# Optimization experiments

Measured on AMD Instinct MI355X. Metric: run time of the kernel, lower is better.

## Reference

```python
import jax, jax.numpy as jnp
import numpy as np

N = 4096      # nodes / sequence length
E = 131072    # edges (avg degree 32)
DIN = 512     # input feature dim
D = 256       # hidden_dim == output_dim (d_model)
H = 2         # nhead
DFF = 2048    # TransformerEncoderLayer default dim_feedforward
EPS = 1e-5


def setup_inputs() -> dict:
    key = jax.random.key(0)
    ks = jax.random.split(key, 16)
    s = lambda k, shape, scale: jax.random.normal(k, shape, jnp.float32) * scale
    return {
        "x": jax.random.normal(ks[0], (N, DIN), jnp.float32),
        "edge_index": jax.random.randint(ks[1], (2, E), 0, N),
        "edge_weight": jax.random.uniform(ks[2], (E,), jnp.float32),
        "W_gcn": s(ks[3], (DIN, D), 1.0 / np.sqrt(DIN)),
        "b_gcn": jnp.zeros((D,), jnp.float32),
        "in_proj_w": s(ks[4], (3 * D, D), 1.0 / np.sqrt(D)),
        "in_proj_b": jnp.zeros((3 * D,), jnp.float32),
        "out_proj_w": s(ks[5], (D, D), 1.0 / np.sqrt(D)),
        "out_proj_b": jnp.zeros((D,), jnp.float32),
        "lin1_w": s(ks[6], (DFF, D), 1.0 / np.sqrt(D)),
        "lin1_b": jnp.zeros((DFF,), jnp.float32),
        "lin2_w": s(ks[7], (D, DFF), 1.0 / np.sqrt(DFF)),
        "lin2_b": jnp.zeros((D,), jnp.float32),
        "ln1_g": jnp.ones((D,), jnp.float32),
        "ln1_b": jnp.zeros((D,), jnp.float32),
        "ln2_g": jnp.ones((D,), jnp.float32),
        "ln2_b": jnp.zeros((D,), jnp.float32),
    }


def _layernorm(x, g, b):
    mu = jnp.mean(x, axis=-1, keepdims=True)
    var = jnp.mean(jnp.square(x - mu), axis=-1, keepdims=True)
    return (x - mu) * jax.lax.rsqrt(var + EPS) * g + b


def _gcn_conv(x, edge_index, edge_weight, W, b):
    # PyG GCNConv: linear transform, add self-loops (weight 1), symmetric
    # degree normalization, scatter-add aggregation at target nodes.
    loops = jnp.arange(N)
    src = jnp.concatenate([edge_index[0], loops])
    dst = jnp.concatenate([edge_index[1], loops])
    w = jnp.concatenate([edge_weight, jnp.ones((N,), edge_weight.dtype)])
    deg = jax.ops.segment_sum(w, dst, num_segments=N)
    dinv = jnp.where(deg > 0, jax.lax.rsqrt(deg), 0.0)
    norm = dinv[src] * w * dinv[dst]                        # [E+N]
    xw = x @ W                                              # [N, D]
    out = jax.ops.segment_sum(norm[:, None] * xw[src], dst, num_segments=N)
    return out + b


def _mha(x, in_w, in_b, out_w, out_b):
    dh = D // H
    qkv = x @ in_w.T + in_b                                 # [N, 3D]
    q, k, v = jnp.split(qkv, 3, axis=-1)
    q = q.reshape(N, H, dh)
    k = k.reshape(N, H, dh)
    v = v.reshape(N, H, dh)
    scores = jnp.einsum("qhd,khd->hqk", q, k) / np.sqrt(dh)  # [H, N, N]
    attn = jax.nn.softmax(scores, axis=-1)
    o = jnp.einsum("hqk,khd->qhd", attn, v).reshape(N, D)
    return o @ out_w.T + out_b


def reference(x, edge_index, edge_weight, W_gcn, b_gcn, in_proj_w, in_proj_b,
              out_proj_w, out_proj_b, lin1_w, lin1_b, lin2_w, lin2_b,
              ln1_g, ln1_b, ln2_g, ln2_b):
    h = jax.nn.relu(_gcn_conv(x, edge_index, edge_weight, W_gcn, b_gcn))
    # TransformerEncoderLayer, post-norm (norm_first=False), dropout=eval
    h = _layernorm(h + _mha(h, in_proj_w, in_proj_b, out_proj_w, out_proj_b),
                   ln1_g, ln1_b)
    ff = jax.nn.relu(h @ lin1_w.T + lin1_b) @ lin2_w.T + lin2_b
    return _layernorm(h + ff, ln2_g, ln2_b)
```

## Files before the change

kernel.cpp:

```cpp
#include <hip/hip_runtime.h>
#include <hip/hip_bf16.h>

#define N_NODES 4096
#define E_EDGES 131072
#define DIN_    512
#define DM_     256
#define DFF_    2048
#define EPS_    1e-5f
#define NSPLIT  8

typedef __attribute__((ext_vector_type(8))) short bf16x8;
typedef __attribute__((ext_vector_type(4))) float f32x4;

__device__ __forceinline__ short f2b(float f) {
    union { float f; unsigned u; } x; x.f = f;
    unsigned r = x.u + 0x7fff + ((x.u >> 16) & 1);
    return (short)(r >> 16);
}

__device__ __forceinline__ void gload16(const void* g, void* l) {
    __builtin_amdgcn_global_load_lds(
        (const __attribute__((address_space(1))) void*)g,
        (__attribute__((address_space(3))) void*)l, 16, 0, 0);
}

__global__ __launch_bounds__(256)
void castall_kernel(const float* __restrict__ x, short* __restrict__ xb,
                    const float* __restrict__ inw, short* __restrict__ inwb,
                    const float* __restrict__ ow, short* __restrict__ owb,
                    const float* __restrict__ l1w, short* __restrict__ l1wb,
                    const float* __restrict__ l2w, short* __restrict__ l2wb,
                    const float* __restrict__ Wg, short* __restrict__ WgT) {
    const int b = blockIdx.x;
    __shared__ float t[32][33];
    if (b >= 3328) {
        const int b2 = b - 3328;
        const int bk = (b2 & 15) * 32, bn = (b2 >> 4) * 32;
        const int tx = threadIdx.x & 31, ty = threadIdx.x >> 5;
        #pragma unroll
        for (int i = 0; i < 4; ++i) {
            int r = ty + i * 8;
            t[r][tx] = Wg[(size_t)(bk + r) * DM_ + bn + tx];
        }
        __syncthreads();
        #pragma unroll
        for (int i = 0; i < 4; ++i) {
            int r = ty + i * 8;
            WgT[(size_t)(bn + r) * DIN_ + bk + tx] = f2b(t[tx][r]);
        }
        return;
    }
    const float* s; short* d; int base;
    if (b < 2048)      { s = x;   d = xb;   base = b * 256; }
    else if (b < 2240) { s = inw; d = inwb; base = (b - 2048) * 256; }
    else if (b < 2304) { s = ow;  d = owb;  base = (b - 2240) * 256; }
    else if (b < 2816) { s = l1w; d = l1wb; base = (b - 2304) * 256; }
    else               { s = l2w; d = l2wb; base = (b - 2816) * 256; }
    const int i = base + threadIdx.x;
    float4 v = reinterpret_cast<const float4*>(s)[i];
    union { short s[4]; int2 v; } o;
    o.s[0] = f2b(v.x); o.s[1] = f2b(v.y); o.s[2] = f2b(v.z); o.s[3] = f2b(v.w);
    reinterpret_cast<int2*>(d)[i] = o.v;
}

template<int MT, bool BF16OUT, bool RELU, bool SPLITK>
__global__ __launch_bounds__(256)
void mgemm_kernel(const short* __restrict__ A, const short* __restrict__ B,
                  const float* __restrict__ bias,
                  float* __restrict__ Cf, short* __restrict__ Cb,
                  short* __restrict__ VTout,
                  int M, int N, int K, int lda, int ldb, int ldc, int kchunk)
{
    constexpr int MFN = MT / 32;
    constexpr int ACH = MT / 64;
    __shared__ __align__(16) short As[2][MT * 32];
    __shared__ __align__(16) short Bs[2][128 * 32];
    const int tid = threadIdx.x;
    const int lane = tid & 63, w = tid >> 6;
    const int c = lane & 15, g = lane >> 4;
    const int wm = (w >> 1) * (MT / 2), wn = (w & 1) * 64;
    const int bm = blockIdx.y * MT, bn = blockIdx.x * 128;
    int k0 = 0, kend = K;
    if (SPLITK) { k0 = blockIdx.z * kchunk; kend = min(K, k0 + kchunk); }

    const int wbase = (tid & ~63) * 16;
    int srowA[ACH], soffA[ACH];
    #pragma unroll
    for (int i = 0; i < ACH; ++i) {
        int L = i * 256 + tid;
        srowA[i] = L >> 2;
        soffA[i] = ((L & 3) ^ ((srowA[i] >> 1) & 3)) * 8;
    }
    int srowB[2], soffB[2];
    #pragma unroll
    for (int i = 0; i < 2; ++i) {
        int L = i * 256 + tid;
        srowB[i] = L >> 2;
        soffB[i] = ((L & 3) ^ ((srowB[i] >> 1) & 3)) * 8;
    }

    auto stage = [&](int b, int kb) {
        #pragma unroll
        for (int i = 0; i < ACH; ++i)
            gload16(A + (size_t)(bm + srowA[i]) * lda + kb + soffA[i],
                    (char*)As[b] + i * 4096 + wbase);
        #pragma unroll
        for (int i = 0; i < 2; ++i)
            gload16(B + (size_t)(bn + srowB[i]) * ldb + kb + soffB[i],
                    (char*)Bs[b] + i * 4096 + wbase);
    };

    const int nsteps = (kend - k0) >> 5;
    f32x4 acc[MFN][4] = {};
    stage(0, k0);
    for (int s = 0; s < nsteps; ++s) {
        const int cur = s & 1;
        const bool pf = (s + 1 < nsteps);
        if (pf) stage(cur ^ 1, k0 + (s + 1) * 32);
        if (pf) {
            if constexpr (ACH == 2) asm volatile("s_waitcnt vmcnt(4)" ::: "memory");
            else                    asm volatile("s_waitcnt vmcnt(3)" ::: "memory");
        } else {
            asm volatile("s_waitcnt vmcnt(0)" ::: "memory");
        }
        __builtin_amdgcn_s_barrier();
        bf16x8 af[MFN], bf[4];
        #pragma unroll
        for (int mf = 0; mf < MFN; ++mf) {
            int r = wm + mf * 16 + c;
            int sw = (g ^ ((r >> 1) & 3)) * 16;
            af[mf] = *reinterpret_cast<const bf16x8*>((const char*)As[cur] + r * 64 + sw);
        }
        #pragma unroll
        for (int nf = 0; nf < 4; ++nf) {
            int r = wn + nf * 16 + c;
            int sw = (g ^ ((r >> 1) & 3)) * 16;
            bf[nf] = *reinterpret_cast<const bf16x8*>((const char*)Bs[cur] + r * 64 + sw);
        }
        #pragma unroll
        for (int mf = 0; mf < MFN; ++mf)
            #pragma unroll
            for (int nf = 0; nf < 4; ++nf)
                acc[mf][nf] = __builtin_amdgcn_mfma_f32_16x16x32_bf16(
                    af[mf], bf[nf], acc[mf][nf], 0, 0, 0);
        __builtin_amdgcn_s_barrier();
    }
    #pragma unroll
    for (int mf = 0; mf < MFN; ++mf) {
        const int row = bm + wm + mf * 16 + g * 4;
        #pragma unroll
        for (int nf = 0; nf < 4; ++nf) {
            const int col = bn + wn + nf * 16 + c;
            float bv = bias ? bias[col] : 0.f;
            #pragma unroll
            for (int v = 0; v < 4; ++v) {
                float val = acc[mf][nf][v];
                size_t o = (size_t)(row + v) * ldc + col;
                if (SPLITK) {
                    if (blockIdx.z == 0) val += bv;
                    atomicAdd(&Cf[o], val);
                } else {
                    val += bv;
                    if (RELU) val = fmaxf(val, 0.f);
                    if (BF16OUT) {
                        short bvs = f2b(val);
                        Cb[o] = bvs;
                        if (VTout && col >= 512)
                            VTout[(size_t)(col - 512) * N_NODES + row + v] = bvs;
                    } else {
                        Cf[o] = val;
                    }
                }
            }
        }
    }
}

__global__ __launch_bounds__(256)
void fattn_kernel(const short* __restrict__ qkv, const short* __restrict__ VT,
                  short* __restrict__ Opart, float* __restrict__ ml)
{
    const int bid = blockIdx.x;
    const int j = bid >> 3;
    const int pair = 2 * (bid & 7) + (j & 1);
    const int hd = pair >> 3, sp = pair & 7;
    const int qt = j >> 1;
    const int tid = threadIdx.x;
    const int w = tid >> 6, lane = tid & 63;
    const int c = lane & 15, g = lane >> 4;
    const int q0 = qt * 64 + w * 16;

    __shared__ __align__(16) char smem[40960];
    char* KldsB = smem;
    char* VldsB = smem + 16384;
    char* Pbase = smem + 32768 + w * 2048;

    const char* qkvC = (const char*)qkv;
    const char* vtC  = (const char*)VT;
    const int wbase = (tid & ~63) * 16;

    const short* Q = qkv + (size_t)q0 * 768 + hd * 128;
    bf16x8 qf[4];
    #pragma unroll
    for (int ks = 0; ks < 4; ++ks)
        qf[ks] = *reinterpret_cast<const bf16x8*>(Q + (size_t)c * 768 + ks * 32 + g * 8);

    auto stageK = [&](int kt) {
        const int key0 = kt * 64;
        #pragma unroll
        for (int i = 0; i < 4; ++i) {
            int Lr  = i * 4096 + tid * 16;
            int key = Lr >> 8;
            int lg  = (Lr & 255) ^ ((key & 7) << 4);
            const char* src = qkvC + ((size_t)(key0 + key) * 768 + 256 + hd * 128) * 2 + lg;
            gload16(src, KldsB + i * 4096 + wbase);
        }
    };
    auto stageV = [&](int kt) {
        const int key0 = kt * 64;
        #pragma unroll
        for (int i = 0; i < 4; ++i) {
            int Lr = i * 4096 + tid * 16;
            int dh = Lr >> 7;
            int lg = (Lr & 127) ^ ((dh & 7) << 4);
            const char* src = vtC + (size_t)(hd * 128 + dh) * 8192 + key0 * 2 + lg;
            gload16(src, VldsB + i * 4096 + wbase);
        }
    };

    f32x4 O[8] = {};
    float m[4]  = {-1e30f, -1e30f, -1e30f, -1e30f};
    float lsum[4] = {};
    const float C = 0.12751744f;

    stageK(sp * 8);
    stageV(sp * 8);

    for (int t = 0; t < 8; ++t) {
        asm volatile("s_waitcnt vmcnt(4)" ::: "memory");
        __builtin_amdgcn_s_barrier();
        f32x4 S[4] = {};
        #pragma unroll
        for (int nf = 0; nf < 4; ++nf) {
            const int key = nf * 16 + c;
            const char* kr = KldsB + key * 256;
            const int sw = (key & 7) << 4;
            #pragma unroll
            for (int ks = 0; ks < 4; ++ks) {
                bf16x8 kf = *reinterpret_cast<const bf16x8*>(kr + ((ks * 64 + g * 16) ^ sw));
                S[nf] = __builtin_amdgcn_mfma_f32_16x16x32_bf16(qf[ks], kf, S[nf], 0, 0, 0);
            }
        }
        __builtin_amdgcn_s_barrier();
        if (t < 7) stageK(sp * 8 + t + 1);

        float z[4][4];
        float lmax[4];
        bool ok = true;
        #pragma unroll
        for (int v = 0; v < 4; ++v) {
            #pragma unroll
            for (int nf = 0; nf < 4; ++nf) z[nf][v] = S[nf][v] * C;
            lmax[v] = fmaxf(fmaxf(z[0][v], z[1][v]), fmaxf(z[2][v], z[3][v]));
            ok = ok && (lmax[v] <= m[v] + 8.f);
        }
        if (!__all(ok)) {
            float mx[4];
            #pragma unroll
            for (int v = 0; v < 4; ++v) mx[v] = lmax[v];
            #pragma unroll
            for (int off = 1; off <= 8; off <<= 1)
                #pragma unroll
                for (int v = 0; v < 4; ++v) mx[v] = fmaxf(mx[v], __shfl_xor(mx[v], off));
            #pragma unroll
            for (int v = 0; v < 4; ++v) {
                float mn = fmaxf(m[v], mx[v]);
                float scl = exp2f(m[v] - mn);
                m[v] = mn;
                lsum[v] *= scl;
                #pragma unroll
                for (int nf2 = 0; nf2 < 8; ++nf2) O[nf2][v] *= scl;
            }
        }
        #pragma unroll
        for (int nf = 0; nf < 4; ++nf)
            #pragma unroll
            for (int v = 0; v < 4; ++v) {
                float p = exp2f(z[nf][v] - m[v]);
                lsum[v] += p;
                union { float f; unsigned u; } pu; pu.f = p;
                const int row = 4 * g + v;
                const int bo = (row * 128 + (nf * 16 + c) * 2) ^ ((row & 7) << 4);
                *(short*)(Pbase + bo) = (short)(pu.u >> 16);
            }
        if (t < 7) asm volatile("s_waitcnt vmcnt(4)" ::: "memory");
        else       asm volatile("s_waitcnt vmcnt(0)" ::: "memory");
        __builtin_amdgcn_s_barrier();
        bf16x8 pa[2];
        #pragma unroll
        for (int ks = 0; ks < 2; ++ks) {
            const int bo = (c * 128 + ks * 64 + g * 16) ^ ((c & 7) << 4);
            pa[ks] = *reinterpret_cast<const bf16x8*>(Pbase + bo);
        }
        #pragma unroll
        for (int nf2 = 0; nf2 < 8; ++nf2) {
            const int dh = nf2 * 16 + c;
            const char* vr = VldsB + dh * 128;
            const int sw = (dh & 7) << 4;
            #pragma unroll
            for (int ks = 0; ks < 2; ++ks) {
                bf16x8 vf = *reinterpret_cast<const bf16x8*>(vr + ((ks * 64 + g * 16) ^ sw));
                O[nf2] = __builtin_amdgcn_mfma_f32_16x16x32_bf16(pa[ks], vf, O[nf2], 0, 0, 0);
            }
        }
        __builtin_amdgcn_s_barrier();
        if (t < 7) stageV(sp * 8 + t + 1);
    }
    #pragma unroll
    for (int off = 1; off <= 8; off <<= 1)
        #pragma unroll
        for (int v = 0; v < 4; ++v) lsum[v] += __shfl_xor(lsum[v], off);
    const size_t pbase = ((size_t)hd * NSPLIT + sp) * N_NODES;
    #pragma unroll
    for (int v = 0; v < 4; ++v) {
        const int row = q0 + 4 * g + v;
        const size_t rowo = (pbase + row) * 128;
        #pragma unroll
        for (int nf2 = 0; nf2 < 8; ++nf2)
            Opart[rowo + nf2 * 16 + c] = f2b(O[nf2][v]);
        if (c == 0) {
            ml[(pbase + row) * 2 + 0] = m[v];
            ml[(pbase + row) * 2 + 1] = lsum[v];
        }
    }
}

__global__ __launch_bounds__(256)
void attn_combine_kernel(const short* __restrict__ Opart, const float* __restrict__ ml,
                         short* __restrict__ attnb)
{
    const int row = blockIdx.x;
    const int hd = threadIdx.x >> 7, d = threadIdx.x & 127;
    float ms[NSPLIT], ls[NSPLIT];
    float mmax = -1e30f;
    #pragma unroll
    for (int s = 0; s < NSPLIT; ++s) {
        const size_t p = ((size_t)hd * NSPLIT + s) * N_NODES + row;
        ms[s] = ml[p * 2 + 0];
        ls[s] = ml[p * 2 + 1];
        mmax = fmaxf(mmax, ms[s]);
    }
    float lt = 0.f, acc = 0.f;
    #pragma unroll
    for (int s = 0; s < NSPLIT; ++s) {
        const float wgt = exp2f(ms[s] - mmax);
        lt += wgt * ls[s];
        const size_t p = ((size_t)hd * NSPLIT + s) * N_NODES + row;
        union { short s; unsigned short u; } b; b.s = Opart[p * 128 + d];
        union { unsigned u; float f; } cv; cv.u = ((unsigned)b.u) << 16;
        acc += wgt * cv.f;
    }
    attnb[(size_t)row * DM_ + hd * 128 + d] = f2b(acc / lt);
}

__global__ void deg_accum_kernel(const int* __restrict__ dst,
                                 const float* __restrict__ w,
                                 float* deg, int* count) {
    int e = blockIdx.x * 256 + threadIdx.x;
    if (e < E_EDGES) {
        int d = dst[e];
        atomicAdd(&deg[d], w[e]);
        atomicAdd(&count[d], 1);
    }
}
__global__ __launch_bounds__(1024)
void csr_scan_kernel(const int* __restrict__ count, int* __restrict__ start,
                     int* __restrict__ cursor, float* __restrict__ deg) {
    __shared__ int sum[1024];
    const int tid = threadIdx.x;
    const int base = tid * 4;
    #pragma unroll
    for (int i = 0; i < 4; ++i) {
        int n = base + i;
        deg[n] = rsqrtf(deg[n] + 1.0f);
    }
    int loc[4]; int s = 0;
    #pragma unroll
    for (int i = 0; i < 4; ++i) { loc[i] = count[base + i]; s += loc[i]; }
    sum[tid] = s;
    __syncthreads();
    for (int off = 1; off < 1024; off <<= 1) {
        int v = (tid >= off) ? sum[tid - off] : 0;
        __syncthreads();
        sum[tid] += v;
        __syncthreads();
    }
    int run = sum[tid] - s;
    #pragma unroll
    for (int i = 0; i < 4; ++i) {
        start[base + i] = run;
        cursor[base + i] = run;
        run += loc[i];
    }
    if (tid == 1023) start[N_NODES] = run;
}
__global__ void csr_fill_kernel(const int* __restrict__ src, const int* __restrict__ dst,
                                const float* __restrict__ w, const float* __restrict__ dinv,
                                int* __restrict__ cursor,
                                int* __restrict__ csr_src, float* __restrict__ csr_nrm) {
    int e = blockIdx.x * 256 + threadIdx.x;
    if (e >= E_EDGES) return;
    int s = src[e], d = dst[e];
    int pos = atomicAdd(&cursor[d], 1);
    csr_src[pos] = s;
    csr_nrm[pos] = dinv[s] * w[e] * dinv[d];
}
__global__ __launch_bounds__(256)
void gcn_gather_kernel(const int* __restrict__ start, const int* __restrict__ csr_src,
                       const float* __restrict__ csr_nrm, const short* __restrict__ xwb,
                       const float* __restrict__ dinv, const float* __restrict__ b,
                       float* __restrict__ h, short* __restrict__ hb) {
    const int n = blockIdx.x, tid = threadIdx.x;
    const int q = tid >> 6, lane = tid & 63;
    const int s0 = start[n], s1 = start[n + 1];
    __shared__ int    ssrc[256];
    __shared__ float  snrm[256];
    __shared__ float4 red[4][64];
    float4 acc = {0.f, 0.f, 0.f, 0.f};
    for (int base = s0; base < s1; base += 256) {
        const int cnt = min(256, s1 - base);
        __syncthreads();
        if (tid < cnt) { ssrc[tid] = csr_src[base + tid]; snrm[tid] = csr_nrm[base + tid]; }
        __syncthreads();
        for (int j = q; j < cnt; j += 4) {
            const int2 pv = *reinterpret_cast<const int2*>(
                xwb + (size_t)ssrc[j] * DM_ + lane * 4);
            union { int i; float f; } e0, e1, e2, e3;
            e0.i = pv.x << 16; e1.i = pv.x & 0xffff0000;
            e2.i = pv.y << 16; e3.i = pv.y & 0xffff0000;
            const float wj = snrm[j];
            acc.x = fmaf(wj, e0.f, acc.x);
            acc.y = fmaf(wj, e1.f, acc.y);
            acc.z = fmaf(wj, e2.f, acc.z);
            acc.w = fmaf(wj, e3.f, acc.w);
        }
    }
    red[q][lane] = acc;
    __syncthreads();
    if (q == 0) {
        const float4 a1 = red[1][lane], a2 = red[2][lane], a3 = red[3][lane];
        const float di = dinv[n], d2 = di * di;
        const int2 pv = *reinterpret_cast<const int2*>(
            xwb + (size_t)n * DM_ + lane * 4);
        union { int i; float f; } x0, x1, x2, x3;
        x0.i = pv.x << 16; x1.i = pv.x & 0xffff0000;
        x2.i = pv.y << 16; x3.i = pv.y & 0xffff0000;
        const float4 bv = *reinterpret_cast<const float4*>(b + lane * 4);
        float v0 = fmaxf(acc.x + a1.x + a2.x + a3.x + d2 * x0.f + bv.x, 0.f);
        float v1 = fmaxf(acc.y + a1.y + a2.y + a3.y + d2 * x1.f + bv.y, 0.f);
        float v2 = fmaxf(acc.z + a1.z + a2.z + a3.z + d2 * x2.f + bv.z, 0.f);
        float v3 = fmaxf(acc.w + a1.w + a2.w + a3.w + d2 * x3.f + bv.w, 0.f);
        const size_t o = (size_t)n * DM_ + lane * 4;
        *reinterpret_cast<float4*>(h + o) = make_float4(v0, v1, v2, v3);
        union { short s[4]; int2 v; } ob;
        ob.s[0] = f2b(v0); ob.s[1] = f2b(v1); ob.s[2] = f2b(v2); ob.s[3] = f2b(v3);
        *reinterpret_cast<int2*>(hb + o) = ob.v;
    }
}

__global__ __launch_bounds__(256)
void ln_kernel(const float* __restrict__ a, const float* __restrict__ b,
               const float* __restrict__ g, const float* __restrict__ be,
               float* __restrict__ outf, short* __restrict__ outb,
               float* __restrict__ clearbuf) {
    const int n = blockIdx.x, d = threadIdx.x;
    const size_t idx = (size_t)n * DM_ + d;
    float x = a[idx] + b[idx];
    if (clearbuf) clearbuf[idx] = 0.f;
    float s = x;
    #pragma unroll
    for (int off = 32; off; off >>= 1) s += __shfl_xor(s, off);
    __shared__ float red[8];
    const int wid = d >> 6;
    if ((d & 63) == 0) red[wid] = s;
    __syncthreads();
    float mu = (red[0] + red[1] + red[2] + red[3]) * (1.f / 256.f);
    float c = x - mu;
    float q = c * c;
    #pragma unroll
    for (int off = 32; off; off >>= 1) q += __shfl_xor(q, off);
    if ((d & 63) == 0) red[4 + wid] = q;
    __syncthreads();
    float var = (red[4] + red[5] + red[6] + red[7]) * (1.f / 256.f);
    float v = c * rsqrtf(var + EPS_) * g[d] + be[d];
    outf[idx] = v;
    if (outb) outb[idx] = f2b(v);
}

extern "C" void kernel_launch(void* const* d_in, const int* in_sizes, int n_in,
                              void* d_out, int out_size, void* d_ws, size_t ws_size,
                              hipStream_t stream) {
    const float* x   = (const float*)d_in[0];
    const int*   ei  = (const int*)  d_in[1];
    const float* ew  = (const float*)d_in[2];
    const float* Wg  = (const float*)d_in[3];
    const float* bg  = (const float*)d_in[4];
    const float* inw = (const float*)d_in[5];
    const float* inb = (const float*)d_in[6];
    const float* ow  = (const float*)d_in[7];
    const float* ob  = (const float*)d_in[8];
    const float* l1w = (const float*)d_in[9];
    const float* l1b = (const float*)d_in[10];
    const float* l2w = (const float*)d_in[11];
    const float* l2b = (const float*)d_in[12];
    const float* g1  = (const float*)d_in[13];
    const float* b1  = (const float*)d_in[14];
    const float* g2  = (const float*)d_in[15];
    const float* b2  = (const float*)d_in[16];
    float* out = (float*)d_out;

    char* ws = (char*)d_ws;
    size_t off = 0;
    auto alloc = [&](size_t bytes) {
        void* p = ws + off;
        off += (bytes + 255) & ~(size_t)255;
        return p;
    };
    float* deg   = (float*)alloc((size_t)N_NODES * 4);
    int*   count = (int*)  alloc((size_t)N_NODES * 4);
    size_t zspan = off;
    float* tmp     = (float*)alloc((size_t)N_NODES * DM_ * 4);
    int*   startA  = (int*)  alloc((size_t)(N_NODES + 1) * 4);
    int*   cursor  = (int*)  alloc((size_t)N_NODES * 4);
    int*   csr_src = (int*)  alloc((size_t)E_EDGES * 4);
    float* csr_nrm = (float*)alloc((size_t)E_EDGES * 4);
    short* xb    = (short*)alloc((size_t)N_NODES * DIN_ * 2);
    short* WgT   = (short*)alloc((size_t)DM_ * DIN_ * 2);
    short* inwb  = (short*)alloc((size_t)768 * DM_ * 2);
    short* owb   = (short*)alloc((size_t)DM_ * DM_ * 2);
    short* l1wb  = (short*)alloc((size_t)DFF_ * DM_ * 2);
    short* l2wb  = (short*)alloc((size_t)DM_ * DFF_ * 2);
    short* xwb   = (short*)alloc((size_t)N_NODES * DM_ * 2);
    float* h     = (float*)alloc((size_t)N_NODES * DM_ * 4);
    short* hb    = (short*)alloc((size_t)N_NODES * DM_ * 2);
    short* qkvb  = (short*)alloc((size_t)N_NODES * 768 * 2);
    short* VT    = (short*)alloc((size_t)DM_ * N_NODES * 2);
    short* attnb = (short*)alloc((size_t)N_NODES * DM_ * 2);
    float* h1    = (float*)alloc((size_t)N_NODES * DM_ * 4);
    short* h1b   = (short*)alloc((size_t)N_NODES * DM_ * 2);
    size_t opart_b = (size_t)2 * NSPLIT * N_NODES * 128 * 2;
    size_t ml_b    = (size_t)2 * NSPLIT * N_NODES * 2 * 4;
    size_t ff1_b   = (size_t)N_NODES * DFF_ * 2;
    char*  R     = (char*)alloc(opart_b + ml_b > ff1_b ? opart_b + ml_b : ff1_b);
    short* Opart = (short*)R;
    float* ml    = (float*)(R + opart_b);
    short* ff1b  = (short*)R;
    (void)ws_size; (void)in_sizes; (void)n_in; (void)out_size;

    const int* srcI = ei;
    const int* dstI = ei + E_EDGES;

    hipMemsetAsync(ws, 0, zspan, stream);
    castall_kernel<<<3456, 256, 0, stream>>>(x, xb, inw, inwb, ow, owb,
                                             l1w, l1wb, l2w, l2wb, Wg, WgT);

    deg_accum_kernel<<<E_EDGES / 256, 256, 0, stream>>>(dstI, ew, deg, count);
    csr_scan_kernel<<<1, 1024, 0, stream>>>(count, startA, cursor, deg);
    csr_fill_kernel<<<E_EDGES / 256, 256, 0, stream>>>(srcI, dstI, ew, deg, cursor,
                                                       csr_src, csr_nrm);
    mgemm_kernel<64, true, false, false><<<dim3(2, 64), 256, 0, stream>>>(
        xb, WgT, nullptr, nullptr, xwb, nullptr,
        N_NODES, DM_, DIN_, DIN_, DIN_, DM_, 0);
    gcn_gather_kernel<<<N_NODES, 256, 0, stream>>>(startA, csr_src, csr_nrm, xwb,
                                                   deg, bg, h, hb);

    mgemm_kernel<64, true, false, false><<<dim3(6, 64), 256, 0, stream>>>(
        hb, inwb, inb, nullptr, qkvb, VT,
        N_NODES, 768, DM_, DM_, DM_, 768, 0);

    fattn_kernel<<<1024, 256, 0, stream>>>(qkvb, VT, Opart, ml);
    attn_combine_kernel<<<N_NODES, 256, 0, stream>>>(Opart, ml, attnb);

    mgemm_kernel<64, false, false, false><<<dim3(2, 64), 256, 0, stream>>>(
        attnb, owb, ob, tmp, nullptr, nullptr,
        N_NODES, DM_, DM_, DM_, DM_, DM_, 0);
    ln_kernel<<<N_NODES, 256, 0, stream>>>(h, tmp, g1, b1, h1, h1b, tmp);

    mgemm_kernel<128, true, true, false><<<dim3(16, 32), 256, 0, stream>>>(
        h1b, l1wb, l1b, nullptr, ff1b, nullptr,
        N_NODES, DFF_, DM_, DM_, DM_, DFF_, 0);
    mgemm_kernel<64, false, false, true><<<dim3(2, 64, 2), 256, 0, stream>>>(
        ff1b, l2wb, l2b, tmp, nullptr, nullptr,
        N_NODES, DM_, DFF_, DFF_, DFF_, DM_, 1024);
    ln_kernel<<<N_NODES, 256, 0, stream>>>(h1, tmp, g2, b2, out, nullptr, nullptr);
}
```

Measured before the change: 173.8 us.

## Drop fp32 residual copies, use wave-per-node GCN gather, fold zeroing into cast

Rewrites the GCN gather so each wavefront handles one node with 4-way unrolled independent loads, removing LDS staging, block-wide syncs and the cross-wave reduction. The fp32 h and h1 buffers are dropped: the layernorm kernels now read the residual from the bf16 copies, which saves global writes and reads at some cost in precision. The memset of deg/count is replaced by an extra block in the cast kernel, removing one launch. The residual path now carries bf16 rounding error that the reference does not have.

```diff
diff --git a/kernel.cpp b/kernel.cpp
--- a/kernel.cpp
+++ b/kernel.cpp
@@ -17,6 +17,10 @@
     unsigned r = x.u + 0x7fff + ((x.u >> 16) & 1);
     return (short)(r >> 16);
 }
+__device__ __forceinline__ float b2f(short s) {
+    union { int i; float f; } v; v.i = ((int)(unsigned short)s) << 16;
+    return v.f;
+}
 
 __device__ __forceinline__ void gload16(const void* g, void* l) {
     __builtin_amdgcn_global_load_lds(
@@ -30,9 +34,18 @@
                     const float* __restrict__ ow, short* __restrict__ owb,
                     const float* __restrict__ l1w, short* __restrict__ l1wb,
                     const float* __restrict__ l2w, short* __restrict__ l2wb,
-                    const float* __restrict__ Wg, short* __restrict__ WgT) {
+                    const float* __restrict__ Wg, short* __restrict__ WgT,
+                    float* __restrict__ deg, int* __restrict__ count) {
     const int b = blockIdx.x;
     __shared__ float t[32][33];
+    if (b == 3456) {
+        #pragma unroll
+        for (int i = 0; i < 16; ++i) {
+            deg[threadIdx.x * 16 + i] = 0.f;
+            count[threadIdx.x * 16 + i] = 0;
+        }
+        return;
+    }
     if (b >= 3328) {
         const int b2 = b - 3328;
         const int bk = (b2 & 15) * 32, bn = (b2 >> 4) * 32;
@@ -419,63 +432,66 @@
 void gcn_gather_kernel(const int* __restrict__ start, const int* __restrict__ csr_src,
                        const float* __restrict__ csr_nrm, const short* __restrict__ xwb,
                        const float* __restrict__ dinv, const float* __restrict__ b,
-                       float* __restrict__ h, short* __restrict__ hb) {
-    const int n = blockIdx.x, tid = threadIdx.x;
-    const int q = tid >> 6, lane = tid & 63;
+                       short* __restrict__ hb) {
+    const int w = threadIdx.x >> 6, lane = threadIdx.x & 63;
+    const int n = blockIdx.x * 4 + w;
     const int s0 = start[n], s1 = start[n + 1];
-    __shared__ int    ssrc[256];
-    __shared__ float  snrm[256];
-    __shared__ float4 red[4][64];
+    const int col = lane * 4;
     float4 acc = {0.f, 0.f, 0.f, 0.f};
-    for (int base = s0; base < s1; base += 256) {
-        const int cnt = min(256, s1 - base);
-        __syncthreads();
-        if (tid < cnt) { ssrc[tid] = csr_src[base + tid]; snrm[tid] = csr_nrm[base + tid]; }
-        __syncthreads();
-        for (int j = q; j < cnt; j += 4) {
-            const int2 pv = *reinterpret_cast<const int2*>(
-                xwb + (size_t)ssrc[j] * DM_ + lane * 4);
+    int j = s0;
+    for (; j + 4 <= s1; j += 4) {
+        int   sj[4]; float wj[4]; int2 vj[4];
+        #pragma unroll
+        for (int u = 0; u < 4; ++u) { sj[u] = csr_src[j + u]; wj[u] = csr_nrm[j + u]; }
+        #pragma unroll
+        for (int u = 0; u < 4; ++u)
+            vj[u] = *reinterpret_cast<const int2*>(xwb + (size_t)sj[u] * DM_ + col);
+        #pragma unroll
+        for (int u = 0; u < 4; ++u) {
             union { int i; float f; } e0, e1, e2, e3;
-            e0.i = pv.x << 16; e1.i = pv.x & 0xffff0000;
-            e2.i = pv.y << 16; e3.i = pv.y & 0xffff0000;
-            const float wj = snrm[j];
-            acc.x = fmaf(wj, e0.f, acc.x);
-            acc.y = fmaf(wj, e1.f, acc.y);
-            acc.z = fmaf(wj, e2.f, acc.z);
-            acc.w = fmaf(wj, e3.f, acc.w);
-        }
-    }
-    red[q][lane] = acc;
-    __syncthreads();
-    if (q == 0) {
-        const float4 a1 = red[1][lane], a2 = red[2][lane], a3 = red[3][lane];
-        const float di = dinv[n], d2 = di * di;
-        const int2 pv = *reinterpret_cast<const int2*>(
-            xwb + (size_t)n * DM_ + lane * 4);
-        union { int i; float f; } x0, x1, x2, x3;
-        x0.i = pv.x << 16; x1.i = pv.x & 0xffff0000;
-        x2.i = pv.y << 16; x3.i = pv.y & 0xffff0000;
-        const float4 bv = *reinterpret_cast<const float4*>(b + lane * 4);
-        float v0 = fmaxf(acc.x + a1.x + a2.x + a3.x + d2 * x0.f + bv.x, 0.f);
-        float v1 = fmaxf(acc.y + a1.y + a2.y + a3.y + d2 * x1.f + bv.y, 0.f);
-        float v2 = fmaxf(acc.z + a1.z + a2.z + a3.z + d2 * x2.f + bv.z, 0.f);
-        float v3 = fmaxf(acc.w + a1.w + a2.w + a3.w + d2 * x3.f + bv.w, 0.f);
-        const size_t o = (size_t)n * DM_ + lane * 4;
-        *reinterpret_cast<float4*>(h + o) = make_float4(v0, v1, v2, v3);
-        union { short s[4]; int2 v; } ob;
-        ob.s[0] = f2b(v0); ob.s[1] = f2b(v1); ob.s[2] = f2b(v2); ob.s[3] = f2b(v3);
-        *reinterpret_cast<int2*>(hb + o) = ob.v;
-    }
+            e0.i = vj[u].x << 16; e1.i = vj[u].x & 0xffff0000;
+            e2.i = vj[u].y << 16; e3.i = vj[u].y & 0xffff0000;
+            acc.x = fmaf(wj[u], e0.f, acc.x);
+            acc.y = fmaf(wj[u], e1.f, acc.y);
+            acc.z = fmaf(wj[u], e2.f, acc.z);
+            acc.w = fmaf(wj[u], e3.f, acc.w);
+        }
+    }
+    for (; j < s1; ++j) {
+        const int sj = csr_src[j];
+        const float wj = csr_nrm[j];
+        const int2 v = *reinterpret_cast<const int2*>(xwb + (size_t)sj * DM_ + col);
+        union { int i; float f; } e0, e1, e2, e3;
+        e0.i = v.x << 16; e1.i = v.x & 0xffff0000;
+        e2.i = v.y << 16; e3.i = v.y & 0xffff0000;
+        acc.x = fmaf(wj, e0.f, acc.x);
+        acc.y = fmaf(wj, e1.f, acc.y);
+        acc.z = fmaf(wj, e2.f, acc.z);
+        acc.w = fmaf(wj, e3.f, acc.w);
+    }
+    const float di = dinv[n], d2 = di * di;
+    const int2 pv = *reinterpret_cast<const int2*>(xwb + (size_t)n * DM_ + col);
+    union { int i; float f; } x0, x1, x2, x3;
+    x0.i = pv.x << 16; x1.i = pv.x & 0xffff0000;
+    x2.i = pv.y << 16; x3.i = pv.y & 0xffff0000;
+    const float4 bv = *reinterpret_cast<const float4*>(b + col);
+    float v0 = fmaxf(acc.x + d2 * x0.f + bv.x, 0.f);
+    float v1 = fmaxf(acc.y + d2 * x1.f + bv.y, 0.f);
+    float v2 = fmaxf(acc.z + d2 * x2.f + bv.z, 0.f);
+    float v3 = fmaxf(acc.w + d2 * x3.f + bv.w, 0.f);
+    union { short s[4]; int2 v; } ob;
+    ob.s[0] = f2b(v0); ob.s[1] = f2b(v1); ob.s[2] = f2b(v2); ob.s[3] = f2b(v3);
+    *reinterpret_cast<int2*>(hb + (size_t)n * DM_ + col) = ob.v;
 }
 
 __global__ __launch_bounds__(256)
-void ln_kernel(const float* __restrict__ a, const float* __restrict__ b,
+void ln_kernel(const short* __restrict__ a, const float* __restrict__ b,
                const float* __restrict__ g, const float* __restrict__ be,
                float* __restrict__ outf, short* __restrict__ outb,
                float* __restrict__ clearbuf) {
     const int n = blockIdx.x, d = threadIdx.x;
     const size_t idx = (size_t)n * DM_ + d;
-    float x = a[idx] + b[idx];
+    float x = b2f(a[idx]) + b[idx];
     if (clearbuf) clearbuf[idx] = 0.f;
     float s = x;
     #pragma unroll
@@ -493,7 +509,7 @@
     __syncthreads();
     float var = (red[4] + red[5] + red[6] + red[7]) * (1.f / 256.f);
     float v = c * rsqrtf(var + EPS_) * g[d] + be[d];
-    outf[idx] = v;
+    if (outf) outf[idx] = v;
     if (outb) outb[idx] = f2b(v);
 }
 
@@ -526,9 +542,8 @@
         off += (bytes + 255) & ~(size_t)255;
         return p;
     };
-    float* deg   = (float*)alloc((size_t)N_NODES * 4);
-    int*   count = (int*)  alloc((size_t)N_NODES * 4);
-    size_t zspan = off;
+    float* deg     = (float*)alloc((size_t)N_NODES * 4);
+    int*   count   = (int*)  alloc((size_t)N_NODES * 4);
     float* tmp     = (float*)alloc((size_t)N_NODES * DM_ * 4);
     int*   startA  = (int*)  alloc((size_t)(N_NODES + 1) * 4);
     int*   cursor  = (int*)  alloc((size_t)N_NODES * 4);
@@ -541,12 +556,10 @@
     short* l1wb  = (short*)alloc((size_t)DFF_ * DM_ * 2);
     short* l2wb  = (short*)alloc((size_t)DM_ * DFF_ * 2);
     short* xwb   = (short*)alloc((size_t)N_NODES * DM_ * 2);
-    float* h     = (float*)alloc((size_t)N_NODES * DM_ * 4);
     short* hb    = (short*)alloc((size_t)N_NODES * DM_ * 2);
     short* qkvb  = (short*)alloc((size_t)N_NODES * 768 * 2);
     short* VT    = (short*)alloc((size_t)DM_ * N_NODES * 2);
     short* attnb = (short*)alloc((size_t)N_NODES * DM_ * 2);
-    float* h1    = (float*)alloc((size_t)N_NODES * DM_ * 4);
     short* h1b   = (short*)alloc((size_t)N_NODES * DM_ * 2);
     size_t opart_b = (size_t)2 * NSPLIT * N_NODES * 128 * 2;
     size_t ml_b    = (size_t)2 * NSPLIT * N_NODES * 2 * 4;
@@ -560,9 +573,9 @@
     const int* srcI = ei;
     const int* dstI = ei + E_EDGES;
 
-    hipMemsetAsync(ws, 0, zspan, stream);
-    castall_kernel<<<3456, 256, 0, stream>>>(x, xb, inw, inwb, ow, owb,
-                                             l1w, l1wb, l2w, l2wb, Wg, WgT);
+    castall_kernel<<<3457, 256, 0, stream>>>(x, xb, inw, inwb, ow, owb,
+                                             l1w, l1wb, l2w, l2wb, Wg, WgT,
+                                             deg, count);
 
     deg_accum_kernel<<<E_EDGES / 256, 256, 0, stream>>>(dstI, ew, deg, count);
     csr_scan_kernel<<<1, 1024, 0, stream>>>(count, startA, cursor, deg);
@@ -571,8 +584,8 @@
     mgemm_kernel<64, true, false, false><<<dim3(2, 64), 256, 0, stream>>>(
         xb, WgT, nullptr, nullptr, xwb, nullptr,
         N_NODES, DM_, DIN_, DIN_, DIN_, DM_, 0);
-    gcn_gather_kernel<<<N_NODES, 256, 0, stream>>>(startA, csr_src, csr_nrm, xwb,
-                                                   deg, bg, h, hb);
+    gcn_gather_kernel<<<1024, 256, 0, stream>>>(startA, csr_src, csr_nrm, xwb,
+                                                deg, bg, hb);
 
     mgemm_kernel<64, true, false, false><<<dim3(6, 64), 256, 0, stream>>>(
         hb, inwb, inb, nullptr, qkvb, VT,
@@ -584,7 +597,7 @@
     mgemm_kernel<64, false, false, false><<<dim3(2, 64), 256, 0, stream>>>(
         attnb, owb, ob, tmp, nullptr, nullptr,
         N_NODES, DM_, DM_, DM_, DM_, DM_, 0);
-    ln_kernel<<<N_NODES, 256, 0, stream>>>(h, tmp, g1, b1, h1, h1b, tmp);
+    ln_kernel<<<N_NODES, 256, 0, stream>>>(hb, tmp, g1, b1, nullptr, h1b, tmp);
 
     mgemm_kernel<128, true, true, false><<<dim3(16, 32), 256, 0, stream>>>(
         h1b, l1wb, l1b, nullptr, ff1b, nullptr,
@@ -592,5 +605,5 @@
     mgemm_kernel<64, false, false, true><<<dim3(2, 64, 2), 256, 0, stream>>>(
         ff1b, l2wb, l2b, tmp, nullptr, nullptr,
         N_NODES, DM_, DFF_, DFF_, DFF_, DM_, 1024);
-    ln_kernel<<<N_NODES, 256, 0, stream>>>(h1, tmp, g2, b2, out, nullptr, nullptr);
-}
+    ln_kernel<<<N_NODES, 256, 0, stream>>>(h1b, tmp, g2, b2, out, nullptr, nullptr);
+}
```

After: 168.9 us. -2.9%, faster.
